# Performance work log

Measured on AMD Instinct MI355X. Metric: run time of the kernel, lower is better.

The kernel has to match this reference:

```python
import jax, jax.numpy as jnp
import numpy as np

# SMPL constants and module defaults
NV, NF, T, S = 6890, 13776, 3, 256
NEAR, FAR = 0.1, 25.0
VIEW_ANGLE = 30.0
EYE = np.array([0.0, 0.0, -(1.0 / np.tan(np.radians(VIEW_ANGLE)) + 1.0)], np.float32)
AMB_INT, DIR_INT = 1.0, 0.0
AMB_COL = np.array([1.0, 1.0, 1.0], np.float32)
DIR_COL = np.array([1.0, 1.0, 1.0], np.float32)
LIGHT_DIR = np.array([0.0, 1.0, 0.0], np.float32)
BG = np.array([0.0, 0.0, 0.0], np.float32)
CHUNK = 128  # faces processed per z-buffer scan step


def _coords(t):
    # create_coords: (2, T*T) barycentric-style grid over [0,1]^2 (torch meshgrid 'ij')
    step = 1.0 / (t - 1) if t > 1 else 1.0
    ab = np.arange(0.0, 1.0 + step * 0.5, step, dtype=np.float32)
    xv, yv = np.meshgrid(ab, ab, indexing='ij')
    return jnp.asarray(np.stack([xv.ravel(), yv.ravel()], 0))

COORDS = _coords(T)


def _grid_sample(img, grid):
    # F.grid_sample: bilinear, zeros padding, align_corners=False
    # img (B,C,H,W), grid (B,N,M,2) in [-1,1] -> (B,C,N,M)
    Bc, C, H, W = img.shape
    gx = (grid[..., 0] + 1.0) * (W * 0.5) - 0.5
    gy = (grid[..., 1] + 1.0) * (H * 0.5) - 0.5
    x0 = jnp.floor(gx)
    y0 = jnp.floor(gy)
    fx = gx - x0
    fy = gy - y0

    def tap(xi, yi, w):
        valid = (xi >= 0) & (xi < W) & (yi >= 0) & (yi < H)
        xc = jnp.clip(xi, 0, W - 1).astype(jnp.int32)
        yc = jnp.clip(yi, 0, H - 1).astype(jnp.int32)
        v = jax.vmap(lambda im, y, x: im[:, y, x])(img, yc, xc)  # (B,C,N,M)
        return v * (w * valid)[:, None]

    return (tap(x0, y0, (1 - fx) * (1 - fy)) + tap(x0 + 1, y0, fx * (1 - fy))
            + tap(x0, y0 + 1, (1 - fx) * fy) + tap(x0 + 1, y0 + 1, fx * fy))


def _rasterize_one(f3, tex):
    # f3: (NF,3,3) camera-space face vertices (x,y in [-1,1] screen, z depth)
    # tex: (NF,T,T,T,3) per-face texture cube. Z-buffer rasterization (NMR-style,
    # CCW front faces only, perspective-correct depth and texture weights).
    F = f3.shape[0]
    pad = (-F) % CHUNK
    f3p = jnp.concatenate([f3, jnp.zeros((pad, 3, 3), f3.dtype)], 0)
    nc = f3p.shape[0] // CHUNK
    chunks = f3p.reshape(nc, CHUNK, 3, 3)
    bases = jnp.arange(nc, dtype=jnp.int32) * CHUNK
    yi, xi = jnp.meshgrid(jnp.arange(S), jnp.arange(S), indexing='ij')
    px = ((2.0 * xi.ravel() + 1.0 - S) / S).astype(f3.dtype)  # (P,)
    py = ((2.0 * yi.ravel() + 1.0 - S) / S).astype(f3.dtype)
    P = S * S

    @jax.checkpoint
    def step(carry, inp):
        zbuf, fid, wbuf = carry
        base, fc = inp
        vx = fc[:, :, 0][..., None]  # (C,3,1)
        vy = fc[:, :, 1][..., None]
        vz = fc[:, :, 2]             # (C,3)
        x0, x1, x2 = vx[:, 0], vx[:, 1], vx[:, 2]
        y0, y1, y2 = vy[:, 0], vy[:, 1], vy[:, 2]
        det = (x1 - x0) * (y2 - y0) - (y1 - y0) * (x2 - x0)  # (C,1)
        e0 = (x1 - px) * (y2 - py) - (y1 - py) * (x2 - px)   # (C,P)
        e1 = (x2 - px) * (y0 - py) - (y2 - py) * (x0 - px)
        e2 = (x0 - px) * (y1 - py) - (y0 - py) * (x1 - px)
        den = jnp.where(jnp.abs(det) > 1e-10, det, 1.0)
        b0, b1, b2 = e0 / den, e1 / den, e2 / den
        zs = jnp.where(jnp.abs(vz) > 1e-8, vz, 1.0)  # (C,3)
        inv_z = b0 / zs[:, 0:1] + b1 / zs[:, 1:2] + b2 / zs[:, 2:3]
        inv_z = jnp.where(jnp.abs(inv_z) > 1e-8, inv_z, 1.0)
        zp = 1.0 / inv_z  # perspective-correct depth at pixel
        inside = (det > 1e-10) & (e0 >= 0) & (e1 >= 0) & (e2 >= 0)
        valid = inside & (zp > NEAR) & (zp < FAR)
        zm = jnp.where(valid, zp, jnp.inf)
        best = jnp.argmin(zm, axis=0)  # (P,)
        bz = jnp.take_along_axis(zm, best[None], 0)[0]
        w = jnp.stack([jnp.take_along_axis(b0, best[None], 0)[0],
                       jnp.take_along_axis(b1, best[None], 0)[0],
                       jnp.take_along_axis(b2, best[None], 0)[0]], -1)  # (P,3)
        zv = zs[best]  # (P,3)
        bzf = jnp.where(jnp.isfinite(bz), bz, 0.0)
        wpc = (w / zv) * bzf[:, None]  # perspective-correct barycentric
        upd = bz < zbuf
        zbuf = jnp.where(upd, bz, zbuf)
        fid = jnp.where(upd, base + best.astype(jnp.int32), fid)
        wbuf = jnp.where(upd[:, None], wpc, wbuf)
        return (zbuf, fid, wbuf), None

    init = (jnp.full((P,), jnp.inf, f3.dtype),
            jnp.full((P,), -1, jnp.int32),
            jnp.zeros((P, 3), f3.dtype))
    (zbuf, fid, wbuf), _ = jax.lax.scan(step, init, (bases, chunks))

    # trilinear texture-cube sampling at barycentric position
    fg = fid >= 0
    fidc = jnp.clip(fid, 0, F - 1)
    pos = jnp.clip(wbuf, 0.0, 1.0) * (T - 1)  # (P,3)
    i0 = jnp.clip(jnp.floor(pos), 0, max(T - 2, 0)).astype(jnp.int32)
    fr = jnp.clip(pos - i0, 0.0, 1.0)
    col = jnp.zeros((P, 3), f3.dtype)
    for d0 in (0, 1):
        for d1 in (0, 1):
            for d2 in (0, 1):
                wgt = ((fr[:, 0] if d0 else 1 - fr[:, 0])
                       * (fr[:, 1] if d1 else 1 - fr[:, 1])
                       * (fr[:, 2] if d2 else 1 - fr[:, 2]))
                c = tex[fidc,
                        jnp.minimum(i0[:, 0] + d0, T - 1),
                        jnp.minimum(i0[:, 1] + d1, T - 1),
                        jnp.minimum(i0[:, 2] + d2, T - 1)]  # (P,3)
                col = col + wgt[:, None] * c
    img = jnp.where(fg[:, None], col, jnp.asarray(BG, f3.dtype))
    return img.reshape(S, S, 3).transpose(2, 0, 1)  # (3,S,S)


def _forward(cam, vertices, uv_imgs, faces):
    B = cam.shape[0]
    # --- dynamic_sampler: orthographic projection + per-face barycentric UV grid ---
    pts2d = cam[:, None, 0:1] * (vertices[:, :, :2] + cam[:, None, 1:3])  # (B,NV,2)
    f2pts = pts2d[:, faces]                                               # (B,NF,3,2)
    v2 = f2pts[:, :, 2]
    mat = jnp.stack([f2pts[:, :, 0] - v2, f2pts[:, :, 1] - v2], axis=-1)  # (B,NF,2,2)
    sampler = jnp.einsum('bfik,kt->bfti', mat, COORDS) + v2[:, :, None, :]
    sampler = jnp.clip(sampler, -1.0, 1.0)                                # (B,NF,T*T,2)
    # --- extract_tex ---
    tex = _grid_sample(uv_imgs, sampler)                                  # (B,3,NF,T*T)
    tex = tex.reshape(B, 3, NF, T, T).transpose(0, 2, 3, 4, 1)            # (B,NF,T,T,3)
    textures = jnp.repeat(tex[:, :, :, :, None, :], T, axis=4)            # (B,NF,T,T,T,3)
    # --- lighting (defaults: ambient=1, directional=0 -> identity; kept general) ---
    fverts = vertices[:, faces]  # (B,NF,3,3)
    n = jnp.cross(fverts[:, :, 1] - fverts[:, :, 0], fverts[:, :, 2] - fverts[:, :, 0])
    n = n / (jnp.linalg.norm(n, axis=-1, keepdims=True) + 1e-10)
    ldir = jnp.asarray(LIGHT_DIR / np.linalg.norm(LIGHT_DIR))
    cos = jax.nn.relu(n @ ldir)
    light = AMB_INT * jnp.asarray(AMB_COL) + DIR_INT * jnp.asarray(DIR_COL) * cos[..., None]
    tex_lit = textures * light[:, :, None, None, None, :]
    # --- projection (y flipped) + look_at ---
    proj = jnp.concatenate([pts2d[..., 0:1], -pts2d[..., 1:2], vertices[:, :, 2:3]], -1)
    eye = jnp.asarray(EYE)
    z_ax = -eye / jnp.linalg.norm(eye)
    x_ax = jnp.cross(jnp.array([0.0, 1.0, 0.0], proj.dtype), z_ax)
    x_ax = x_ax / jnp.linalg.norm(x_ax)
    y_ax = jnp.cross(z_ax, x_ax)
    R = jnp.stack([x_ax, y_ax, z_ax])  # (3,3)
    vcam = (proj - eye) @ R.T
    f3 = vcam[:, faces]  # (B,NF,3,3)
    images = jax.vmap(_rasterize_one)(f3, tex_lit)  # (B,3,S,S)
    return images, textures


def setup_inputs() -> dict:
    key = jax.random.key(0)
    k1, k2, k3, k4 = jax.random.split(key, 4)
    cam = jax.random.uniform(k1, (1, 3), dtype=jnp.float32)
    vertices = jax.random.normal(k2, (1, NV, 3), dtype=jnp.float32)
    uv_imgs = jax.random.uniform(k3, (1, 3, 256, 256), dtype=jnp.float32)
    faces = jax.random.randint(k4, (NF, 3), 0, NV, dtype=jnp.int32)
    return {"cam": cam, "vertices": vertices, "uv_imgs": uv_imgs, "faces": faces}


def reference(cam, vertices, uv_imgs, faces):
    return _forward(cam, vertices, uv_imgs, faces)
```

## Files before the change

kernel.cpp:

```cpp
#include <hip/hip_runtime.h>

#define NVERT 6890
#define NFACE 13776
#define SS 256
#define NPIX (SS*SS)
#define TILE 8
#define NSB 256
#define SPLIT 16
#define SEGLEN 861
#define SENTINEL 0x7F800000FFFFFFFFULL

#define OFF_KEYS 0u
#define OFF_VB   524288u
#define OFF_FD   607232u
#define OFF_TD   1488896u

static __device__ __forceinline__ float edgef(float ax, float ay, float bx, float by,
                                              float px, float py) {
  return __fsub_rn(__fmul_rn(__fsub_rn(ax, px), __fsub_rn(by, py)),
                   __fmul_rn(__fsub_rn(ay, py), __fsub_rn(bx, px)));
}

__global__ __launch_bounds__(256) void vert_k(const float* __restrict__ cam,
                                              const float* __restrict__ verts,
                                              float* __restrict__ vb) {
  int i = blockIdx.x * 256 + threadIdx.x;
  if (i >= NVERT) return;
  float c0 = cam[0], c1 = cam[1], c2 = cam[2];
  float vx = verts[i*3+0], vy = verts[i*3+1], vz = verts[i*3+2];
  vb[i*3+0] = __fmul_rn(c0, __fadd_rn(vx, c1));
  vb[i*3+1] = __fmul_rn(c0, __fadd_rn(vy, c2));
  vb[i*3+2] = __fadd_rn(vz, 2.7320508075688776f);
}

__global__ __launch_bounds__(256) void init_k(unsigned long long* __restrict__ keys) {
  int p = blockIdx.x * 256 + threadIdx.x;
  if (p < NPIX) keys[p] = SENTINEL;
}

__global__ __launch_bounds__(256) void tex_k(const float* __restrict__ vb,
                                             const int* __restrict__ faces,
                                             const float* __restrict__ uv,
                                             float* __restrict__ out_tex) {
  int tid = blockIdx.x * 256 + threadIdx.x;
  if (tid >= NFACE * 9) return;
  int f = tid / 9, t = tid - f * 9;
  int ti = t / 3, tj = t - ti * 3;
  float xt = 0.5f * (float)ti;
  float yt = 0.5f * (float)tj;
  int ia = faces[f*3+0], ib = faces[f*3+1], ic = faces[f*3+2];
  float ax = vb[ia*3+0], ay = vb[ia*3+1];
  float bx = vb[ib*3+0], by = vb[ib*3+1];
  float cx = vb[ic*3+0], cy = vb[ic*3+1];
  float sx = (ax - cx) * xt + (bx - cx) * yt + cx;
  float sy = (ay - cy) * xt + (by - cy) * yt + cy;
  sx = fminf(fmaxf(sx, -1.f), 1.f);
  sy = fminf(fmaxf(sy, -1.f), 1.f);
  float gx = (sx + 1.f) * 128.f - 0.5f;
  float gy = (sy + 1.f) * 128.f - 0.5f;
  float x0f = floorf(gx), y0f = floorf(gy);
  float fx = gx - x0f, fy = gy - y0f;
  int x0 = (int)x0f, y0 = (int)y0f;
  float r = 0.f, g = 0.f, b = 0.f;
  #pragma unroll
  for (int dy = 0; dy < 2; ++dy) {
    #pragma unroll
    for (int dx = 0; dx < 2; ++dx) {
      int xi = x0 + dx, yi = y0 + dy;
      if (xi >= 0 && xi < SS && yi >= 0 && yi < SS) {
        float w = (dx ? fx : 1.f - fx) * (dy ? fy : 1.f - fy);
        int base = yi * SS + xi;
        r += w * uv[base];
        g += w * uv[NPIX + base];
        b += w * uv[2 * NPIX + base];
      }
    }
  }
  float* ot = out_tex + f * 81 + ti * 27 + tj * 9;
  #pragma unroll
  for (int kk = 0; kk < 3; ++kk) {
    ot[kk*3+0] = r; ot[kk*3+1] = g; ot[kk*3+2] = b;
  }
}

__global__ __launch_bounds__(256) void setup_k(const float* __restrict__ vb,
                                               const int* __restrict__ faces,
                                               float* __restrict__ fd,
                                               uint2* __restrict__ td) {
  int f = blockIdx.x * 256 + threadIdx.x;
  if (f >= NFACE) return;
  float* fp = fd + (size_t)f * 16;
  int ia = faces[f*3+0], ib = faces[f*3+1], ic = faces[f*3+2];
  float x0 = vb[ia*3+0], y0 = -vb[ia*3+1], z0 = vb[ia*3+2];
  float x1 = vb[ib*3+0], y1 = -vb[ib*3+1], z1 = vb[ib*3+2];
  float x2 = vb[ic*3+0], y2 = -vb[ic*3+1], z2 = vb[ic*3+2];
  float det = edgef(x1, y1, x2, y2, x0, y0);
  unsigned int tilepack = 0x000000FFu;
  if (det > 1e-10f) {
    float mnx = fminf(x0, fminf(x1, x2)), mxx = fmaxf(x0, fmaxf(x1, x2));
    float mny = fminf(y0, fminf(y1, y2)), mxy = fmaxf(y0, fmaxf(y1, y2));
    int xlo = max((int)floorf((mnx * 256.f + 255.f) * 0.5f) - 2, 0);
    int xhi = min((int)ceilf ((mxx * 256.f + 255.f) * 0.5f) + 2, SS - 1);
    int ylo = max((int)floorf((mny * 256.f + 255.f) * 0.5f) - 2, 0);
    int yhi = min((int)ceilf ((mxy * 256.f + 255.f) * 0.5f) + 2, SS - 1);
    if (xlo <= xhi && ylo <= yhi)
      tilepack = (unsigned int)(xlo >> 3) | ((unsigned int)(ylo >> 3) << 8)
               | ((unsigned int)(xhi >> 3) << 16) | ((unsigned int)(yhi >> 3) << 24);
  }
  float rz0 = (fabsf(z0) > 1e-8f) ? z0 : 1.0f;
  float rz1 = (fabsf(z1) > 1e-8f) ? z1 : 1.0f;
  float rz2 = (fabsf(z2) > 1e-8f) ? z2 : 1.0f;
  float minrz = fminf(fminf(fabsf(rz0), fabsf(rz1)), fabsf(rz2));
  unsigned int flag = (minrz < 0.05f) ? 1u : 0u;
  unsigned int zmb = 0u;
  if (flag == 0u) {
    float mn = fminf(fminf(rz0, rz1), rz2);
    if (mn > 0.f) zmb = __float_as_uint(mn * 0.999f);
  }
  fp[0] = x0;  fp[1] = y0;  fp[2] = x1;  fp[3] = y1;
  fp[4] = x2;  fp[5] = y2;  fp[6] = rz0; fp[7] = rz1;
  fp[8] = rz2; fp[9] = det;
  fp[10] = __fdiv_rn(1.0f, det * rz0);
  fp[11] = __fdiv_rn(1.0f, det * rz1);
  fp[12] = __fdiv_rn(1.0f, det * rz2);
  fp[13] = __uint_as_float((unsigned int)f | (flag << 24));
  fp[14] = __uint_as_float(tilepack);
  fp[15] = __uint_as_float(zmb);
  td[f] = make_uint2(tilepack, zmb);
}

__global__ __launch_bounds__(256) void tile_k(const float* __restrict__ fd,
                                              const uint2* __restrict__ td,
                                              unsigned long long* __restrict__ keys) {
  __shared__ unsigned short idx_s[4][256];
  __shared__ unsigned int cnt_s[4];
  __shared__ unsigned int wmax_s[4];
  int sb  = blockIdx.x & (NSB - 1);
  int seg = blockIdx.x >> 8;
  int tid = threadIdx.x;
  int w = tid >> 6, lane = tid & 63;
  int sbx = sb & 15, sby = sb >> 4;
  int tx = sbx * 2 + (w & 1);
  int ty = sby * 2 + (w >> 1);
  int xx = tx * TILE + (lane & 7);
  int yy = ty * TILE + (lane >> 3);
  float px = (float)(2 * xx + 1 - SS) * (1.0f / 256.0f);
  float py = (float)(2 * yy + 1 - SS) * (1.0f / 256.0f);
  unsigned long long best = SENTINEL;
  int fbeg = seg * SEGLEN;
  int fend = min(fbeg + SEGLEN, NFACE);

  for (int base = fbeg; base < fend; base += 256) {
    unsigned int bh = (unsigned int)(best >> 32);
    #pragma unroll
    for (int o = 32; o > 0; o >>= 1)
      bh = max(bh, (unsigned int)__shfl_xor((int)bh, o, 64));
    __syncthreads();
    if (lane == 0) wmax_s[w] = bh;
    if (tid < 4) cnt_s[tid] = 0;
    __syncthreads();
    int f = base + tid;
    if (f < fend) {
      uint2 t2 = td[f];
      unsigned int tp = t2.x, zmb = t2.y;
      int tx0 = (int)(tp & 255u),         ty0 = (int)((tp >> 8) & 255u);
      int tx1 = (int)((tp >> 16) & 255u), ty1 = (int)(tp >> 24);
      #pragma unroll
      for (int q = 0; q < 4; ++q) {
        int qtx = sbx * 2 + (q & 1);
        int qty = sby * 2 + (q >> 1);
        if (qtx >= tx0 && qtx <= tx1 && qty >= ty0 && qty <= ty1
            && zmb <= wmax_s[q]) {
          unsigned int slot = atomicAdd(&cnt_s[q], 1u);
          idx_s[q][slot] = (unsigned short)f;
        }
      }
    }
    __syncthreads();
    int m = (int)cnt_s[w];
    for (int j = 0; j < m; ++j) {
      int f2 = __builtin_amdgcn_readfirstlane((int)idx_s[w][j]);
      const float4* fr = (const float4*)(fd + (size_t)f2 * 16);
      float4 A  = fr[0];
      float4 Bv = fr[1];
      float4 Cv = fr[2];
      float4 Dv = fr[3];
      unsigned int zmb = __float_as_uint(Dv.w);
      if (zmb > (unsigned int)(best >> 32)) continue;
      float e0 = edgef(A.z, A.w, Bv.x, Bv.y, px, py);
      float e1 = edgef(Bv.x, Bv.y, A.x, A.y, px, py);
      float e2 = edgef(A.x, A.y, A.z, A.w, px, py);
      if (e0 >= 0.f && e1 >= 0.f && e2 >= 0.f) {
        float inva = __fmaf_rn(e0, Cv.z, __fmaf_rn(e1, Cv.w, e2 * Dv.x));
        float zc = __uint_as_float((unsigned int)(best >> 32));
        unsigned int w13 = __float_as_uint(Dv.y);
        bool pass = ((w13 >> 24) != 0u) | (inva * zc > 0.998f) | (fabsf(inva) < 1e-4f);
        if (pass) {
          float rz0 = Bv.z, rz1 = Bv.w, rz2 = Cv.x, det = Cv.y;
          float b0 = __fdiv_rn(e0, det);
          float b1 = __fdiv_rn(e1, det);
          float b2 = __fdiv_rn(e2, det);
          float inv = __fadd_rn(__fadd_rn(__fdiv_rn(b0, rz0), __fdiv_rn(b1, rz1)),
                                __fdiv_rn(b2, rz2));
          if (!(fabsf(inv) > 1e-8f)) inv = 1.0f;
          float zp = __fdiv_rn(1.0f, inv);
          if (zp > 0.1f && zp < 25.0f) {
            unsigned long long key =
                ((unsigned long long)__float_as_uint(zp) << 32)
                | (w13 & 0x00FFFFFFu);
            if (key < best) best = key;
          }
        }
      }
    }
  }
  if (best != SENTINEL) {
    int p = yy * SS + xx;
    if (best < keys[p]) atomicMin(&keys[p], best);
  }
}

__global__ __launch_bounds__(256) void resolve_k(const float* __restrict__ vb,
                                                 const int* __restrict__ faces,
                                                 const unsigned long long* __restrict__ keys,
                                                 const float* __restrict__ out_tex,
                                                 float* __restrict__ out_img) {
  int p = blockIdx.x * 256 + threadIdx.x;
  if (p >= NPIX) return;
  unsigned long long k = keys[p];
  float c0 = 0.f, c1 = 0.f, c2 = 0.f;
  if (k != SENTINEL) {
    int f = (int)(unsigned int)(k & 0x00FFFFFFULL);
    float bz = __uint_as_float((unsigned int)(k >> 32));
    int xx = p & (SS - 1), yy = p >> 8;
    float px = (float)(2 * xx + 1 - SS) * (1.0f / 256.0f);
    float py = (float)(2 * yy + 1 - SS) * (1.0f / 256.0f);
    int ia = faces[f*3+0], ib = faces[f*3+1], ic = faces[f*3+2];
    float x0 = vb[ia*3+0], y0 = -vb[ia*3+1], z0 = vb[ia*3+2];
    float x1 = vb[ib*3+0], y1 = -vb[ib*3+1], z1 = vb[ib*3+2];
    float x2 = vb[ic*3+0], y2 = -vb[ic*3+1], z2 = vb[ic*3+2];
    float det = edgef(x1, y1, x2, y2, x0, y0);
    float e0 = edgef(x1, y1, x2, y2, px, py);
    float e1 = edgef(x2, y2, x0, y0, px, py);
    float e2 = edgef(x0, y0, x1, y1, px, py);
    float b0 = __fdiv_rn(e0, det);
    float b1 = __fdiv_rn(e1, det);
    float b2 = __fdiv_rn(e2, det);
    float rz0 = (fabsf(z0) > 1e-8f) ? z0 : 1.0f;
    float rz1 = (fabsf(z1) > 1e-8f) ? z1 : 1.0f;
    float rz2 = (fabsf(z2) > 1e-8f) ? z2 : 1.0f;
    float w0 = __fmul_rn(__fdiv_rn(b0, rz0), bz);
    float w1 = __fmul_rn(__fdiv_rn(b1, rz1), bz);
    float w2 = __fmul_rn(__fdiv_rn(b2, rz2), bz);
    float pos0 = fminf(fmaxf(w0, 0.f), 1.f) * 2.f;
    float pos1 = fminf(fmaxf(w1, 0.f), 1.f) * 2.f;
    float pos2 = fminf(fmaxf(w2, 0.f), 1.f) * 2.f;
    float i0f = fminf(fmaxf(floorf(pos0), 0.f), 1.f);
    float i1f = fminf(fmaxf(floorf(pos1), 0.f), 1.f);
    float i2f = fminf(fmaxf(floorf(pos2), 0.f), 1.f);
    float fr0 = fminf(fmaxf(__fsub_rn(pos0, i0f), 0.f), 1.f);
    float fr1 = fminf(fmaxf(__fsub_rn(pos1, i1f), 0.f), 1.f);
    float fr2 = fminf(fmaxf(__fsub_rn(pos2, i2f), 0.f), 1.f);
    int i00 = (int)i0f, i01 = (int)i1f;
    #pragma unroll
    for (int d0 = 0; d0 < 2; ++d0) {
      float wa = d0 ? fr0 : __fsub_rn(1.f, fr0);
      #pragma unroll
      for (int d1 = 0; d1 < 2; ++d1) {
        float wb = d1 ? fr1 : __fsub_rn(1.f, fr1);
        int a = min(i00 + d0, 2);
        int b = min(i01 + d1, 2);
        const float* tp = &out_tex[f * 81 + a * 27 + b * 9];
        float wab = __fmul_rn(wa, wb);
        #pragma unroll
        for (int d2 = 0; d2 < 2; ++d2) {
          float wc = d2 ? fr2 : __fsub_rn(1.f, fr2);
          float wgt = __fmul_rn(wab, wc);
          c0 = __fadd_rn(c0, __fmul_rn(wgt, tp[0]));
          c1 = __fadd_rn(c1, __fmul_rn(wgt, tp[1]));
          c2 = __fadd_rn(c2, __fmul_rn(wgt, tp[2]));
        }
      }
    }
  }
  out_img[p]          = c0;
  out_img[NPIX + p]   = c1;
  out_img[2*NPIX + p] = c2;
}

extern "C" void kernel_launch(void* const* d_in, const int* in_sizes, int n_in,
                              void* d_out, int out_size, void* d_ws, size_t ws_size,
                              hipStream_t stream) {
  const float* cam   = (const float*)d_in[0];
  const float* verts = (const float*)d_in[1];
  const float* uv    = (const float*)d_in[2];
  const int*   faces = (const int*)d_in[3];
  float* out_img = (float*)d_out;
  float* out_tex = (float*)d_out + 3 * NPIX;

  char* ws = (char*)d_ws;
  unsigned long long* keys = (unsigned long long*)(ws + OFF_KEYS);
  float* vb = (float*)(ws + OFF_VB);
  float* fd = (float*)(ws + OFF_FD);
  uint2* td = (uint2*)(ws + OFF_TD);

  vert_k<<<(NVERT + 255) / 256, 256, 0, stream>>>(cam, verts, vb);
  init_k<<<NPIX / 256, 256, 0, stream>>>(keys);
  tex_k<<<(NFACE * 9 + 255) / 256, 256, 0, stream>>>(vb, faces, uv, out_tex);
  setup_k<<<(NFACE + 255) / 256, 256, 0, stream>>>(vb, faces, fd, td);
  tile_k<<<NSB * SPLIT, 256, 0, stream>>>(fd, td, keys);
  resolve_k<<<NPIX / 256, 256, 0, stream>>>(vb, faces, keys, out_tex, out_img);
}
```

Baseline: 156.1 us.

## Depth-sort faces into buckets and early-exit tile passes using the global z-buffer

Faces are bucketed by their minimum depth using a histogram, a prefix scan and a scatter. The scatter interleaves them across the 16 segments so each segment sees faces from near to far. Each tile pass reads the current global key per pixel, uses it to tighten culling, and breaks out once the segment's next depth bucket lies beyond every pixel's current depth. Partial results are published through atomicMin after each chunk so other segments can cull more. The vertex-prep and key-init kernels are merged into one. Two small extra kernels and more global atomics are added, and traversal order now depends on dynamic cross-block state.

Measured after the change: 190.9 us. 22.3% more time.

```diff
diff --git a/kernel.cpp b/kernel.cpp
--- a/kernel.cpp
+++ b/kernel.cpp
@@ -9,11 +9,18 @@
 #define SPLIT 16
 #define SEGLEN 861
 #define SENTINEL 0x7F800000FFFFFFFFULL
+#define ZBASE 0x3D000000u
 
 #define OFF_KEYS 0u
 #define OFF_VB   524288u
 #define OFF_FD   607232u
-#define OFF_TD   1488896u
+#define OFF_HIST 1488896u
+#define OFF_CURS 1489920u
+#define OFF_TD2  1490944u
+
+static __device__ __forceinline__ unsigned int zbucket(unsigned int zmb) {
+  return (zmb > ZBASE) ? min(255u, (zmb - ZBASE) >> 19) : 0u;
+}
 
 static __device__ __forceinline__ float edgef(float ax, float ay, float bx, float by,
                                               float px, float py) {
@@ -21,21 +28,21 @@
                    __fmul_rn(__fsub_rn(ay, py), __fsub_rn(bx, px)));
 }
 
-__global__ __launch_bounds__(256) void vert_k(const float* __restrict__ cam,
+__global__ __launch_bounds__(256) void prep_k(const float* __restrict__ cam,
                                               const float* __restrict__ verts,
-                                              float* __restrict__ vb) {
+                                              float* __restrict__ vb,
+                                              unsigned long long* __restrict__ keys,
+                                              unsigned int* __restrict__ hist) {
   int i = blockIdx.x * 256 + threadIdx.x;
-  if (i >= NVERT) return;
-  float c0 = cam[0], c1 = cam[1], c2 = cam[2];
-  float vx = verts[i*3+0], vy = verts[i*3+1], vz = verts[i*3+2];
-  vb[i*3+0] = __fmul_rn(c0, __fadd_rn(vx, c1));
-  vb[i*3+1] = __fmul_rn(c0, __fadd_rn(vy, c2));
-  vb[i*3+2] = __fadd_rn(vz, 2.7320508075688776f);
-}
-
-__global__ __launch_bounds__(256) void init_k(unsigned long long* __restrict__ keys) {
-  int p = blockIdx.x * 256 + threadIdx.x;
-  if (p < NPIX) keys[p] = SENTINEL;
+  keys[i] = SENTINEL;
+  if (i < 256) hist[i] = 0u;
+  if (i < NVERT) {
+    float c0 = cam[0], c1 = cam[1], c2 = cam[2];
+    float vx = verts[i*3+0], vy = verts[i*3+1], vz = verts[i*3+2];
+    vb[i*3+0] = __fmul_rn(c0, __fadd_rn(vx, c1));
+    vb[i*3+1] = __fmul_rn(c0, __fadd_rn(vy, c2));
+    vb[i*3+2] = __fadd_rn(vz, 2.7320508075688776f);
+  }
 }
 
 __global__ __launch_bounds__(256) void tex_k(const float* __restrict__ vb,
@@ -86,7 +93,7 @@
 __global__ __launch_bounds__(256) void setup_k(const float* __restrict__ vb,
                                                const int* __restrict__ faces,
                                                float* __restrict__ fd,
-                                               uint2* __restrict__ td) {
+                                               unsigned int* __restrict__ hist) {
   int f = blockIdx.x * 256 + threadIdx.x;
   if (f >= NFACE) return;
   float* fp = fd + (size_t)f * 16;
@@ -126,11 +133,40 @@
   fp[13] = __uint_as_float((unsigned int)f | (flag << 24));
   fp[14] = __uint_as_float(tilepack);
   fp[15] = __uint_as_float(zmb);
-  td[f] = make_uint2(tilepack, zmb);
+  atomicAdd(&hist[zbucket(zmb)], 1u);
+}
+
+__global__ __launch_bounds__(256) void bscan_k(const unsigned int* __restrict__ hist,
+                                               unsigned int* __restrict__ curs) {
+  __shared__ unsigned int bsh[256];
+  int tid = threadIdx.x;
+  unsigned int v = hist[tid];
+  bsh[tid] = v;
+  __syncthreads();
+  for (int off = 1; off < 256; off <<= 1) {
+    unsigned int t = (tid >= off) ? bsh[tid - off] : 0u;
+    __syncthreads();
+    bsh[tid] += t;
+    __syncthreads();
+  }
+  curs[tid] = bsh[tid] - v;
+}
+
+__global__ __launch_bounds__(256) void scatter_k(const float* __restrict__ fd,
+                                                 unsigned int* __restrict__ curs,
+                                                 uint4* __restrict__ td2) {
+  int f = blockIdx.x * 256 + threadIdx.x;
+  if (f >= NFACE) return;
+  const float* fp = fd + (size_t)f * 16;
+  unsigned int tilepack = __float_as_uint(fp[14]);
+  unsigned int zmb      = __float_as_uint(fp[15]);
+  unsigned int slot = atomicAdd(&curs[zbucket(zmb)], 1u);
+  unsigned int pos = (slot & 15u) * SEGLEN + (slot >> 4);
+  td2[pos] = make_uint4(tilepack, zmb, (unsigned int)f, 0u);
 }
 
 __global__ __launch_bounds__(256) void tile_k(const float* __restrict__ fd,
-                                              const uint2* __restrict__ td,
+                                              const uint4* __restrict__ td2,
                                               unsigned long long* __restrict__ keys) {
   __shared__ unsigned short idx_s[4][256];
   __shared__ unsigned int cnt_s[4];
@@ -146,12 +182,15 @@
   int yy = ty * TILE + (lane >> 3);
   float px = (float)(2 * xx + 1 - SS) * (1.0f / 256.0f);
   float py = (float)(2 * yy + 1 - SS) * (1.0f / 256.0f);
+  int p = yy * SS + xx;
   unsigned long long best = SENTINEL;
-  int fbeg = seg * SEGLEN;
-  int fend = min(fbeg + SEGLEN, NFACE);
-
-  for (int base = fbeg; base < fend; base += 256) {
-    unsigned int bh = (unsigned int)(best >> 32);
+  unsigned long long lastw = SENTINEL;
+  const uint4* tseg = td2 + (size_t)seg * SEGLEN;
+
+  for (int base = 0; base < SEGLEN; base += 256) {
+    unsigned int gz = (unsigned int)(keys[p] >> 32);
+    unsigned int kz = min((unsigned int)(best >> 32), gz);
+    unsigned int bh = kz;
     #pragma unroll
     for (int o = 32; o > 0; o >>= 1)
       bh = max(bh, (unsigned int)__shfl_xor((int)bh, o, 64));
@@ -159,9 +198,14 @@
     if (lane == 0) wmax_s[w] = bh;
     if (tid < 4) cnt_s[tid] = 0;
     __syncthreads();
-    int f = base + tid;
-    if (f < fend) {
-      uint2 t2 = td[f];
+    unsigned int bm = max(max(wmax_s[0], wmax_s[1]), max(wmax_s[2], wmax_s[3]));
+    unsigned int z0 = tseg[base].y;
+    unsigned int b0 = zbucket(z0);
+    unsigned int lb = b0 ? (ZBASE + (b0 << 19)) : 0u;
+    if (lb > bm) break;
+    int fi = base + tid;
+    if (fi < SEGLEN) {
+      uint4 t2 = tseg[fi];
       unsigned int tp = t2.x, zmb = t2.y;
       int tx0 = (int)(tp & 255u),         ty0 = (int)((tp >> 8) & 255u);
       int tx1 = (int)((tp >> 16) & 255u), ty1 = (int)(tp >> 24);
@@ -172,7 +216,7 @@
         if (qtx >= tx0 && qtx <= tx1 && qty >= ty0 && qty <= ty1
             && zmb <= wmax_s[q]) {
           unsigned int slot = atomicAdd(&cnt_s[q], 1u);
-          idx_s[q][slot] = (unsigned short)f;
+          idx_s[q][slot] = (unsigned short)t2.z;
         }
       }
     }
@@ -186,37 +230,40 @@
       float4 Cv = fr[2];
       float4 Dv = fr[3];
       unsigned int zmb = __float_as_uint(Dv.w);
-      if (zmb > (unsigned int)(best >> 32)) continue;
+      if (zmb > kz) continue;
       float e0 = edgef(A.z, A.w, Bv.x, Bv.y, px, py);
       float e1 = edgef(Bv.x, Bv.y, A.x, A.y, px, py);
       float e2 = edgef(A.x, A.y, A.z, A.w, px, py);
       if (e0 >= 0.f && e1 >= 0.f && e2 >= 0.f) {
         float inva = __fmaf_rn(e0, Cv.z, __fmaf_rn(e1, Cv.w, e2 * Dv.x));
-        float zc = __uint_as_float((unsigned int)(best >> 32));
+        float zc = __uint_as_float(kz);
         unsigned int w13 = __float_as_uint(Dv.y);
         bool pass = ((w13 >> 24) != 0u) | (inva * zc > 0.998f) | (fabsf(inva) < 1e-4f);
         if (pass) {
           float rz0 = Bv.z, rz1 = Bv.w, rz2 = Cv.x, det = Cv.y;
-          float b0 = __fdiv_rn(e0, det);
-          float b1 = __fdiv_rn(e1, det);
-          float b2 = __fdiv_rn(e2, det);
-          float inv = __fadd_rn(__fadd_rn(__fdiv_rn(b0, rz0), __fdiv_rn(b1, rz1)),
-                                __fdiv_rn(b2, rz2));
+          float b0f = __fdiv_rn(e0, det);
+          float b1f = __fdiv_rn(e1, det);
+          float b2f = __fdiv_rn(e2, det);
+          float inv = __fadd_rn(__fadd_rn(__fdiv_rn(b0f, rz0), __fdiv_rn(b1f, rz1)),
+                                __fdiv_rn(b2f, rz2));
           if (!(fabsf(inv) > 1e-8f)) inv = 1.0f;
           float zp = __fdiv_rn(1.0f, inv);
           if (zp > 0.1f && zp < 25.0f) {
             unsigned long long key =
                 ((unsigned long long)__float_as_uint(zp) << 32)
                 | (w13 & 0x00FFFFFFu);
-            if (key < best) best = key;
+            if (key < best) {
+              best = key;
+              kz = min(kz, (unsigned int)(best >> 32));
+            }
           }
         }
       }
     }
-  }
-  if (best != SENTINEL) {
-    int p = yy * SS + xx;
-    if (best < keys[p]) atomicMin(&keys[p], best);
+    if (best != lastw && (unsigned int)(best >> 32) <= gz) {
+      atomicMin(&keys[p], best);
+      lastw = best;
+    }
   }
 }
 
@@ -300,14 +347,17 @@
 
   char* ws = (char*)d_ws;
   unsigned long long* keys = (unsigned long long*)(ws + OFF_KEYS);
-  float* vb = (float*)(ws + OFF_VB);
-  float* fd = (float*)(ws + OFF_FD);
-  uint2* td = (uint2*)(ws + OFF_TD);
-
-  vert_k<<<(NVERT + 255) / 256, 256, 0, stream>>>(cam, verts, vb);
-  init_k<<<NPIX / 256, 256, 0, stream>>>(keys);
+  float* vb          = (float*)(ws + OFF_VB);
+  float* fd          = (float*)(ws + OFF_FD);
+  unsigned int* hist = (unsigned int*)(ws + OFF_HIST);
+  unsigned int* curs = (unsigned int*)(ws + OFF_CURS);
+  uint4* td2         = (uint4*)(ws + OFF_TD2);
+
+  prep_k<<<NPIX / 256, 256, 0, stream>>>(cam, verts, vb, keys, hist);
   tex_k<<<(NFACE * 9 + 255) / 256, 256, 0, stream>>>(vb, faces, uv, out_tex);
-  setup_k<<<(NFACE + 255) / 256, 256, 0, stream>>>(vb, faces, fd, td);
-  tile_k<<<NSB * SPLIT, 256, 0, stream>>>(fd, td, keys);
+  setup_k<<<(NFACE + 255) / 256, 256, 0, stream>>>(vb, faces, fd, hist);
+  bscan_k<<<1, 256, 0, stream>>>(hist, curs);
+  scatter_k<<<(NFACE + 255) / 256, 256, 0, stream>>>(fd, curs, td2);
+  tile_k<<<NSB * SPLIT, 256, 0, stream>>>(fd, td2, keys);
   resolve_k<<<NPIX / 256, 256, 0, stream>>>(vb, faces, keys, out_tex, out_img);
 }
```
